# Performance work log

Measured on AMD Instinct MI355X. Metric: run time of the kernel, lower is better.

## Reference

```python
import jax, jax.numpy as jnp
import numpy as np

L, B = 1024, 64
VALID_FRAC = 0.9  # fraction of residues with nonzero (observed) coordinates in y


def setup_inputs() -> dict:
    key = jax.random.key(0)
    kx, ky = jax.random.split(key)
    x = jax.random.normal(kx, (L, B, 3), dtype=jnp.float32)
    y = jax.random.normal(ky, (L, B, 3), dtype=jnp.float32)
    # zero out trailing residues in y so the dynamic mask (co.sum() != 0) is exercised
    valid = (jnp.arange(L) < int(VALID_FRAC * L))[:, None, None]
    y = y * valid.astype(jnp.float32)
    return {"x": x, "y": y}


def _masked_pair_dist(pts, pair_mask):
    # pts: [B, L, 3]; pair_mask: [B, L, L] (False on diagonal and on padded rows/cols)
    sq = jnp.sum(pts * pts, axis=-1)                                   # [B, L]
    d2 = sq[:, :, None] + sq[:, None, :] - 2.0 * jnp.einsum('bld,bmd->blm', pts, pts)
    d2 = jnp.maximum(d2, 0.0)                                          # relu, matches F.relu
    safe = jnp.where(pair_mask, d2, 1.0)                               # keep sqrt grad finite
    return jnp.where(pair_mask, jnp.sqrt(safe), 0.0)


def reference(x, y):
    # x, y: [L, B, 3] -> permute to [B, L, 3] as in the torch module
    xb = jnp.transpose(x, (1, 0, 2))
    yb = jnp.transpose(y, (1, 0, 2))
    Bn, Ln = xb.shape[0], xb.shape[1]
    # mask: residues of y whose coordinate sum is nonzero (index_select in original)
    mask = (jnp.sum(yb, axis=-1) != 0)                                 # [B, L]
    off_diag = ~jnp.eye(Ln, dtype=bool)
    pair_mask = mask[:, :, None] & mask[:, None, :] & off_diag         # [B, L, L]
    xd = _masked_pair_dist(xb, pair_mask)
    yd = _masked_pair_dist(yb, pair_mask)
    D = yd - xd                                                        # [B, L, L]
    per_batch = jnp.sqrt(jnp.sum(D * D, axis=(1, 2)))                  # Frobenius norm per batch
    denom = (Ln ** 2 / 2 - Ln) ** 0.5                                  # x.size(1)**2/2 - x.size(1)
    out = jnp.sum(per_batch) / denom / Bn
    return out.reshape(1)
```

## Files before the change

### kernel.cpp

```cpp
#include <hip/hip_runtime.h>
#include <math.h>

#define Lp 1024
#define Bp 64
#define Tt 128
#define NTILE 8
#define NPAIR 36

typedef float v4f __attribute__((ext_vector_type(4)));
static __device__ __forceinline__ v4f splat4(float s) {
    v4f r; r.x = s; r.y = s; r.z = s; r.w = s; return r;
}

__global__ __launch_bounds__(256) void drmsd_main(
    const float* __restrict__ x, const float* __restrict__ y,
    float* __restrict__ partials)
{
    __shared__ __align__(16) float xsx[2][Tt], xsy[2][Tt], xsz[2][Tt];
    __shared__ __align__(16) float ysx[2][Tt], ysy[2][Tt], ysz[2][Tt];
    __shared__ __align__(16) float ms[2][Tt];
    __shared__ float red[4];

    const int b = blockIdx.x;
    const int p = blockIdx.y;

    int ti = 0, base = 0;
    while (p >= base + (NTILE - ti)) { base += (NTILE - ti); ++ti; }
    const int tj = ti + (p - base);

    const int t = threadIdx.x;

    {
        const int r     = t & (Tt - 1);
        const int which = t >> 7;
        const int tile  = which ? tj : ti;
        const int row   = tile * Tt + r;
        const float* px = x + (size_t)row * (Bp * 3) + (size_t)b * 3;
        const float* py = y + (size_t)row * (Bp * 3) + (size_t)b * 3;
        const float x0 = px[0], x1 = px[1], x2 = px[2];
        const float y0 = py[0], y1 = py[1], y2 = py[2];
        xsx[which][r] = x0; xsy[which][r] = x1; xsz[which][r] = x2;
        ysx[which][r] = y0; ysy[which][r] = y1; ysz[which][r] = y2;
        ms[which][r]  = ((y0 + y1 + y2) != 0.0f) ? 1.0f : 0.0f;
    }
    __syncthreads();

    const int jsl = (t & 7) << 2;
    const int rg  = t >> 3;
    const int i0  = rg << 2;
    const int wv  = t >> 6;

    const float4 v_xx = *(const float4*)&xsx[0][i0];
    const float4 v_xy = *(const float4*)&xsy[0][i0];
    const float4 v_xz = *(const float4*)&xsz[0][i0];
    const float4 v_yx = *(const float4*)&ysx[0][i0];
    const float4 v_yy = *(const float4*)&ysy[0][i0];
    const float4 v_yz = *(const float4*)&ysz[0][i0];
    const float4 v_mi = *(const float4*)&ms[0][i0];
    const float xix[4] = { v_xx.x, v_xx.y, v_xx.z, v_xx.w };
    const float xiy[4] = { v_xy.x, v_xy.y, v_xy.z, v_xy.w };
    const float xiz[4] = { v_xz.x, v_xz.y, v_xz.z, v_xz.w };
    const float yix[4] = { v_yx.x, v_yx.y, v_yx.z, v_yx.w };
    const float yiy[4] = { v_yy.x, v_yy.y, v_yy.z, v_yy.w };
    const float yiz[4] = { v_yz.x, v_yz.y, v_yz.z, v_yz.w };
    const float mir[4] = { v_mi.x, v_mi.y, v_mi.z, v_mi.w };

    v4f acc[4];
#pragma unroll
    for (int r = 0; r < 4; ++r) acc[r] = splat4(0.0f);

    const v4f neg2 = splat4(-2.0f);

#pragma unroll
    for (int jj = 0; jj < 4; ++jj) {
        const int j0 = jj * 32 + jsl;
        const v4f xjx = *(const v4f*)&xsx[1][j0];
        const v4f xjy = *(const v4f*)&xsy[1][j0];
        const v4f xjz = *(const v4f*)&xsz[1][j0];
        const v4f yjx = *(const v4f*)&ysx[1][j0];
        const v4f yjy = *(const v4f*)&ysy[1][j0];
        const v4f yjz = *(const v4f*)&ysz[1][j0];
        const v4f mj  = *(const v4f*)&ms[1][j0];
#pragma unroll
        for (int r = 0; r < 4; ++r) {
            const v4f ax = splat4(xix[r]) - xjx;
            const v4f ay = splat4(xiy[r]) - xjy;
            const v4f az = splat4(xiz[r]) - xjz;
            const v4f d2x = ax * ax + ay * ay + az * az;
            const v4f bx = splat4(yix[r]) - yjx;
            const v4f by = splat4(yiy[r]) - yjy;
            const v4f bz = splat4(yiz[r]) - yjz;
            const v4f d2y = bx * bx + by * by + bz * bz;
            const v4f pr = d2x * d2y;
            v4f sq;
            sq.x = __builtin_amdgcn_sqrtf(pr.x);
            sq.y = __builtin_amdgcn_sqrtf(pr.y);
            sq.z = __builtin_amdgcn_sqrtf(pr.z);
            sq.w = __builtin_amdgcn_sqrtf(pr.w);
            const v4f u = (d2x + d2y) + neg2 * sq;
            acc[r] = mj * u + acc[r];
        }
    }

    float total = 0.0f;
#pragma unroll
    for (int r = 0; r < 4; ++r)
        total = fmaf(acc[r].x + acc[r].y + acc[r].z + acc[r].w, mir[r], total);

#pragma unroll
    for (int off = 32; off > 0; off >>= 1)
        total += __shfl_down(total, off, 64);
    if ((t & 63) == 0) red[wv] = total;
    __syncthreads();
    if (t == 0) {
        float s = red[0] + red[1] + red[2] + red[3];
        if (ti != tj) s *= 2.0f;
        partials[(size_t)p * Bp + b] = s;
    }
}

__global__ __launch_bounds__(256) void drmsd_final(
    const float* __restrict__ partials, float* __restrict__ out)
{
    __shared__ float sums[256];
    const int t    = threadIdx.x;
    const int lane = t & 63;
    const int q    = t >> 6;
    float s = 0.0f;
#pragma unroll
    for (int k = 0; k < 9; ++k) {
        const int pidx = q * 9 + k;
        s += partials[(size_t)pidx * Bp + lane];
    }
    sums[t] = s;
    __syncthreads();
    if (t < 64) {
        float v = sums[t] + sums[t + 64] + sums[t + 128] + sums[t + 192];
        float pb = sqrtf(v);
#pragma unroll
        for (int off = 32; off > 0; off >>= 1)
            pb += __shfl_down(pb, off, 64);
        if (t == 0) {
            const double denom = sqrt((double)Lp * (double)Lp / 2.0 - (double)Lp);
            out[0] = (float)((double)pb / denom / (double)Bp);
        }
    }
}

extern "C" void kernel_launch(void* const* d_in, const int* in_sizes, int n_in,
                              void* d_out, int out_size, void* d_ws, size_t ws_size,
                              hipStream_t stream) {
    const float* x = (const float*)d_in[0];
    const float* y = (const float*)d_in[1];
    float* out      = (float*)d_out;
    float* partials = (float*)d_ws;

    dim3 grid(Bp, NPAIR);
    drmsd_main<<<grid, 256, 0, stream>>>(x, y, partials);
    drmsd_final<<<1, 256, 0, stream>>>(partials, out);
}
```

Measured before the change: 73.69 us.

## Replace per-pair squared-distance sums with closed-form moment statistics and packed FP32 math

The sums of d2x and d2y over all masked pairs are now computed in closed form from per-tile moments (count, sum of squared norms, coordinate sums), gathered in diagonal blocks and combined in the final kernel. This leaves only the sqrt(d2x*d2y) cross term in the inner loop. The remaining inner-loop arithmetic uses v_pk_add/mul/fma_f32 inline asm on pre-negated, duplicated j coordinates. The trade-off is cancellation in the moment formula, which subtracts large numbers in FP32, and extra shuffle reductions in diagonal blocks.

```diff
diff --git a/kernel.cpp b/kernel.cpp
--- a/kernel.cpp
+++ b/kernel.cpp
@@ -7,19 +7,30 @@
 #define NTILE 8
 #define NPAIR 36
 
-typedef float v4f __attribute__((ext_vector_type(4)));
-static __device__ __forceinline__ v4f splat4(float s) {
-    v4f r; r.x = s; r.y = s; r.z = s; r.w = s; return r;
+typedef float v2f __attribute__((ext_vector_type(2)));
+
+static __device__ __forceinline__ v2f pk_add(v2f a, v2f b) {
+    v2f d; asm("v_pk_add_f32 %0, %1, %2" : "=v"(d) : "v"(a), "v"(b)); return d;
+}
+static __device__ __forceinline__ v2f pk_mul(v2f a, v2f b) {
+    v2f d; asm("v_pk_mul_f32 %0, %1, %2" : "=v"(d) : "v"(a), "v"(b)); return d;
+}
+static __device__ __forceinline__ v2f pk_fma(v2f a, v2f b, v2f c) {
+    v2f d; asm("v_pk_fma_f32 %0, %1, %2, %3" : "=v"(d) : "v"(a), "v"(b), "v"(c)); return d;
 }
 
 __global__ __launch_bounds__(256) void drmsd_main(
     const float* __restrict__ x, const float* __restrict__ y,
-    float* __restrict__ partials)
+    float* __restrict__ partials, float* __restrict__ statsbuf)
 {
-    __shared__ __align__(16) float xsx[2][Tt], xsy[2][Tt], xsz[2][Tt];
-    __shared__ __align__(16) float ysx[2][Tt], ysy[2][Tt], ysz[2][Tt];
-    __shared__ __align__(16) float ms[2][Tt];
+    __shared__ __align__(16) float xs0x[Tt], xs0y[Tt], xs0z[Tt];
+    __shared__ __align__(16) float ys0x[Tt], ys0y[Tt], ys0z[Tt];
+    __shared__ __align__(16) float ms0[Tt];
+    __shared__ __align__(16) float nx1x[2*Tt], nx1y[2*Tt], nx1z[2*Tt];
+    __shared__ __align__(16) float ny1x[2*Tt], ny1y[2*Tt], ny1z[2*Tt];
+    __shared__ __align__(16) float ms1[Tt];
     __shared__ float red[4];
+    __shared__ float sred[2][9];
 
     const int b = blockIdx.x;
     const int p = blockIdx.y;
@@ -39,73 +50,108 @@
         const float* py = y + (size_t)row * (Bp * 3) + (size_t)b * 3;
         const float x0 = px[0], x1 = px[1], x2 = px[2];
         const float y0 = py[0], y1 = py[1], y2 = py[2];
-        xsx[which][r] = x0; xsy[which][r] = x1; xsz[which][r] = x2;
-        ysx[which][r] = y0; ysy[which][r] = y1; ysz[which][r] = y2;
-        ms[which][r]  = ((y0 + y1 + y2) != 0.0f) ? 1.0f : 0.0f;
+        const float m  = ((y0 + y1 + y2) != 0.0f) ? 1.0f : 0.0f;
+        if (which) {
+            const int rd = r << 1;
+            nx1x[rd] = -x0; nx1x[rd+1] = -x0;
+            nx1y[rd] = -x1; nx1y[rd+1] = -x1;
+            nx1z[rd] = -x2; nx1z[rd+1] = -x2;
+            ny1x[rd] = -y0; ny1x[rd+1] = -y0;
+            ny1y[rd] = -y1; ny1y[rd+1] = -y1;
+            ny1z[rd] = -y2; ny1z[rd+1] = -y2;
+            ms1[r] = m;
+        } else {
+            xs0x[r] = x0; xs0y[r] = x1; xs0z[r] = x2;
+            ys0x[r] = y0; ys0y[r] = y1; ys0z[r] = y2;
+            ms0[r] = m;
+        }
+        if (ti == tj && !which) {
+            float c[9];
+            c[0] = m;
+            c[1] = m * (x0*x0 + x1*x1 + x2*x2);
+            c[2] = m * x0; c[3] = m * x1; c[4] = m * x2;
+            c[5] = m * (y0*y0 + y1*y1 + y2*y2);
+            c[6] = m * y0; c[7] = m * y1; c[8] = m * y2;
+#pragma unroll
+            for (int k = 0; k < 9; ++k) {
+                float v = c[k];
+#pragma unroll
+                for (int off = 32; off > 0; off >>= 1)
+                    v += __shfl_down(v, off, 64);
+                c[k] = v;
+            }
+            if ((t & 63) == 0) {
+#pragma unroll
+                for (int k = 0; k < 9; ++k) sred[t >> 6][k] = c[k];
+            }
+        }
     }
     __syncthreads();
+
+    if (ti == tj && t == 0) {
+        float* sb = statsbuf + ((size_t)b * NTILE + ti) * 9;
+#pragma unroll
+        for (int k = 0; k < 9; ++k) sb[k] = sred[0][k] + sred[1][k];
+    }
 
     const int jsl = (t & 7) << 2;
     const int rg  = t >> 3;
     const int i0  = rg << 2;
     const int wv  = t >> 6;
 
-    const float4 v_xx = *(const float4*)&xsx[0][i0];
-    const float4 v_xy = *(const float4*)&xsy[0][i0];
-    const float4 v_xz = *(const float4*)&xsz[0][i0];
-    const float4 v_yx = *(const float4*)&ysx[0][i0];
-    const float4 v_yy = *(const float4*)&ysy[0][i0];
-    const float4 v_yz = *(const float4*)&ysz[0][i0];
-    const float4 v_mi = *(const float4*)&ms[0][i0];
-    const float xix[4] = { v_xx.x, v_xx.y, v_xx.z, v_xx.w };
-    const float xiy[4] = { v_xy.x, v_xy.y, v_xy.z, v_xy.w };
-    const float xiz[4] = { v_xz.x, v_xz.y, v_xz.z, v_xz.w };
-    const float yix[4] = { v_yx.x, v_yx.y, v_yx.z, v_yx.w };
-    const float yiy[4] = { v_yy.x, v_yy.y, v_yy.z, v_yy.w };
-    const float yiz[4] = { v_yz.x, v_yz.y, v_yz.z, v_yz.w };
-    const float mir[4] = { v_mi.x, v_mi.y, v_mi.z, v_mi.w };
-
-    v4f acc[4];
-#pragma unroll
-    for (int r = 0; r < 4; ++r) acc[r] = splat4(0.0f);
-
-    const v4f neg2 = splat4(-2.0f);
+    const float4 fxx = *(const float4*)&xs0x[i0];
+    const float4 fxy = *(const float4*)&xs0y[i0];
+    const float4 fxz = *(const float4*)&xs0z[i0];
+    const float4 fyx = *(const float4*)&ys0x[i0];
+    const float4 fyy = *(const float4*)&ys0y[i0];
+    const float4 fyz = *(const float4*)&ys0z[i0];
+    const float4 fmi = *(const float4*)&ms0[i0];
+    v2f Ax[2], Ay[2], Az[2], Bx[2], By[2], Bz[2];
+    Ax[0] = (v2f){fxx.x, fxx.y}; Ax[1] = (v2f){fxx.z, fxx.w};
+    Ay[0] = (v2f){fxy.x, fxy.y}; Ay[1] = (v2f){fxy.z, fxy.w};
+    Az[0] = (v2f){fxz.x, fxz.y}; Az[1] = (v2f){fxz.z, fxz.w};
+    Bx[0] = (v2f){fyx.x, fyx.y}; Bx[1] = (v2f){fyx.z, fyx.w};
+    By[0] = (v2f){fyy.x, fyy.y}; By[1] = (v2f){fyy.z, fyy.w};
+    Bz[0] = (v2f){fyz.x, fyz.y}; Bz[1] = (v2f){fyz.z, fyz.w};
+
+    float acc[4] = {0.f, 0.f, 0.f, 0.f};
 
 #pragma unroll
     for (int jj = 0; jj < 4; ++jj) {
-        const int j0 = jj * 32 + jsl;
-        const v4f xjx = *(const v4f*)&xsx[1][j0];
-        const v4f xjy = *(const v4f*)&xsy[1][j0];
-        const v4f xjz = *(const v4f*)&xsz[1][j0];
-        const v4f yjx = *(const v4f*)&ysx[1][j0];
-        const v4f yjy = *(const v4f*)&ysy[1][j0];
-        const v4f yjz = *(const v4f*)&ysz[1][j0];
-        const v4f mj  = *(const v4f*)&ms[1][j0];
-#pragma unroll
-        for (int r = 0; r < 4; ++r) {
-            const v4f ax = splat4(xix[r]) - xjx;
-            const v4f ay = splat4(xiy[r]) - xjy;
-            const v4f az = splat4(xiz[r]) - xjz;
-            const v4f d2x = ax * ax + ay * ay + az * az;
-            const v4f bx = splat4(yix[r]) - yjx;
-            const v4f by = splat4(yiy[r]) - yjy;
-            const v4f bz = splat4(yiz[r]) - yjz;
-            const v4f d2y = bx * bx + by * by + bz * bz;
-            const v4f pr = d2x * d2y;
-            v4f sq;
-            sq.x = __builtin_amdgcn_sqrtf(pr.x);
-            sq.y = __builtin_amdgcn_sqrtf(pr.y);
-            sq.z = __builtin_amdgcn_sqrtf(pr.z);
-            sq.w = __builtin_amdgcn_sqrtf(pr.w);
-            const v4f u = (d2x + d2y) + neg2 * sq;
-            acc[r] = mj * u + acc[r];
-        }
-    }
-
+#pragma unroll
+        for (int c = 0; c < 4; ++c) {
+            const int j  = jj * 32 + jsl + c;
+            const int jd = j << 1;
+            const v2f njx = *(const v2f*)&nx1x[jd];
+            const v2f njy = *(const v2f*)&nx1y[jd];
+            const v2f njz = *(const v2f*)&nx1z[jd];
+            const v2f mjx = *(const v2f*)&ny1x[jd];
+            const v2f mjy = *(const v2f*)&ny1y[jd];
+            const v2f mjz = *(const v2f*)&ny1z[jd];
+            const float mj = ms1[j];
+#pragma unroll
+            for (int rp = 0; rp < 2; ++rp) {
+                const v2f ax = pk_add(Ax[rp], njx);
+                const v2f ay = pk_add(Ay[rp], njy);
+                const v2f az = pk_add(Az[rp], njz);
+                const v2f d2x = pk_fma(ax, ax, pk_fma(ay, ay, pk_mul(az, az)));
+                const v2f bx = pk_add(Bx[rp], mjx);
+                const v2f by = pk_add(By[rp], mjy);
+                const v2f bz = pk_add(Bz[rp], mjz);
+                const v2f d2y = pk_fma(bx, bx, pk_fma(by, by, pk_mul(bz, bz)));
+                const v2f pr = pk_mul(d2x, d2y);
+                const float s0 = __builtin_amdgcn_sqrtf(pr.x);
+                const float s1 = __builtin_amdgcn_sqrtf(pr.y);
+                acc[rp*2]   = fmaf(mj, s0, acc[rp*2]);
+                acc[rp*2+1] = fmaf(mj, s1, acc[rp*2+1]);
+            }
+        }
+    }
+
+    const float mir[4] = { fmi.x, fmi.y, fmi.z, fmi.w };
     float total = 0.0f;
 #pragma unroll
-    for (int r = 0; r < 4; ++r)
-        total = fmaf(acc[r].x + acc[r].y + acc[r].z + acc[r].w, mir[r], total);
+    for (int r = 0; r < 4; ++r) total = fmaf(acc[r], mir[r], total);
 
 #pragma unroll
     for (int off = 32; off > 0; off >>= 1)
@@ -120,7 +166,8 @@
 }
 
 __global__ __launch_bounds__(256) void drmsd_final(
-    const float* __restrict__ partials, float* __restrict__ out)
+    const float* __restrict__ partials, const float* __restrict__ statsbuf,
+    float* __restrict__ out)
 {
     __shared__ float sums[256];
     const int t    = threadIdx.x;
@@ -135,8 +182,20 @@
     sums[t] = s;
     __syncthreads();
     if (t < 64) {
-        float v = sums[t] + sums[t + 64] + sums[t + 128] + sums[t + 192];
-        float pb = sqrtf(v);
+        const int bb = t;
+        const float cross = sums[t] + sums[t + 64] + sums[t + 128] + sums[t + 192];
+        float st[9] = {0.f,0.f,0.f,0.f,0.f,0.f,0.f,0.f,0.f};
+#pragma unroll
+        for (int tile = 0; tile < NTILE; ++tile) {
+            const float* sb = statsbuf + ((size_t)bb * NTILE + tile) * 9;
+#pragma unroll
+            for (int k = 0; k < 9; ++k) st[k] += sb[k];
+        }
+        const float nv  = st[0];
+        const float sepx = 2.0f * (nv * st[1] - (st[2]*st[2] + st[3]*st[3] + st[4]*st[4]));
+        const float sepy = 2.0f * (nv * st[5] - (st[6]*st[6] + st[7]*st[7] + st[8]*st[8]));
+        const float Sb = fmaxf(sepx + sepy - 2.0f * cross, 0.0f);
+        float pb = sqrtf(Sb);
 #pragma unroll
         for (int off = 32; off > 0; off >>= 1)
             pb += __shfl_down(pb, off, 64);
@@ -154,8 +213,9 @@
     const float* y = (const float*)d_in[1];
     float* out      = (float*)d_out;
     float* partials = (float*)d_ws;
+    float* statsbuf = (float*)((char*)d_ws + 9216);
 
     dim3 grid(Bp, NPAIR);
-    drmsd_main<<<grid, 256, 0, stream>>>(x, y, partials);
-    drmsd_final<<<1, 256, 0, stream>>>(partials, out);
-}
+    drmsd_main<<<grid, 256, 0, stream>>>(x, y, partials, statsbuf);
+    drmsd_final<<<1, 256, 0, stream>>>(partials, statsbuf, out);
+}
```

After: 76.43 us. 3.7% more time.
